# Performance work log

Hardware: AMD Instinct MI355X
Metric: run time of the kernel (lower is better)

## Reference

```python
import jax, jax.numpy as jnp
import numpy as np
import math

H = 16
DQ = 64
NEG = -1000000000.0


def setup_inputs() -> dict:
    key = jax.random.key(0)
    ks = jax.random.split(key, 8)
    B, S, D = 2, 2048, 1024
    scale = 1.0 / math.sqrt(D)
    return {
        "embedding": jax.random.normal(ks[0], (B, S, D), dtype=jnp.float32),
        "mask": jax.random.randint(ks[1], (B, 1, S), 0, 2, dtype=jnp.int32),
        "Wq": jax.random.normal(ks[2], (D, D), dtype=jnp.float32) * scale,
        "bq": jnp.zeros((D,), dtype=jnp.float32),
        "Wk": jax.random.normal(ks[3], (D, D), dtype=jnp.float32) * scale,
        "bk": jnp.zeros((D,), dtype=jnp.float32),
        "Wv": jax.random.normal(ks[4], (D, D), dtype=jnp.float32) * scale,
        "bv": jnp.zeros((D,), dtype=jnp.float32),
        "Wo": jax.random.normal(ks[5], (D, D), dtype=jnp.float32) * scale,
        "bo": jnp.zeros((D,), dtype=jnp.float32),
    }


def reference(embedding, mask, Wq, bq, Wk, bk, Wv, bv, Wo, bo):
    B, S, D = embedding.shape
    # projections -> [B, H, S, DQ]
    def proj(W, b):
        return (embedding @ W + b).reshape(B, S, H, DQ).transpose(0, 2, 1, 3)
    q, k, v = proj(Wq, bq), proj(Wk, bk), proj(Wv, bv)
    scores = jnp.einsum("bhqd,bhkd->bhqk", q, k) / math.sqrt(DQ)
    m = mask[:, None]  # [B,1,1,S] broadcasts over heads and query positions
    scores = jnp.where(m == 0, NEG, scores)
    attn = jax.nn.softmax(scores, axis=-1)
    x = jnp.einsum("bhqk,bhkd->bhqd", attn, v)
    x = x.transpose(0, 2, 1, 3).reshape(B, S, H * DQ)
    return x @ Wo + bo
```

## Files before the change

### kernel.cpp

```cpp
#include <hip/hip_runtime.h>
#include <stdint.h>

#define B_ 2
#define S_ 2048
#define D_ 1024
#define H_ 16
#define DQ_ 64
#define M_ 4096
#define CLOG2 16.0f

typedef unsigned short ushort_t;
typedef __attribute__((ext_vector_type(8))) short short8;
typedef __attribute__((ext_vector_type(4))) float floatx4;
typedef __attribute__((ext_vector_type(16))) float floatx16;

#if __has_builtin(__builtin_amdgcn_exp2f)
#define EXP2(x) __builtin_amdgcn_exp2f(x)
#else
#define EXP2(x) exp2f(x)
#endif

__device__ __forceinline__ ushort_t f2bf(float f) {
  union { float f; uint32_t u; } v; v.f = f;
  uint32_t r = v.u + 0x7FFFu + ((v.u >> 16) & 1u);
  return (ushort_t)(r >> 16);
}

__device__ __forceinline__ uint32_t pk2_trunc(float a, float b) {
  union { float f; uint32_t u; } va, vb; va.f = a; vb.f = b;
  return (va.u >> 16) | (vb.u & 0xFFFF0000u);
}
__device__ __forceinline__ uint32_t pk2_rne(float a, float b) {
  return (uint32_t)f2bf(a) | ((uint32_t)f2bf(b) << 16);
}

__device__ __forceinline__ void async16(const ushort_t* g, ushort_t* l) {
  __builtin_amdgcn_global_load_lds(
      (const __attribute__((address_space(1))) uint32_t*)g,
      (__attribute__((address_space(3))) uint32_t*)l, 16, 0, 0);
}


__global__ void k_cvt_emb(const float* __restrict__ in, ushort_t* __restrict__ out) {
  int i = (blockIdx.x * 256 + threadIdx.x) * 4;
  float4 v = *(const float4*)(in + i);
  uint64_t pk = (uint64_t)f2bf(v.x) | ((uint64_t)f2bf(v.y) << 16) |
                ((uint64_t)f2bf(v.z) << 32) | ((uint64_t)f2bf(v.w) << 48);
  *(uint64_t*)(out + i) = pk;
}

__global__ void k_cvt_w(const float* __restrict__ Wq, const float* __restrict__ Wk,
                        const float* __restrict__ Wv, const float* __restrict__ Wo,
                        ushort_t* __restrict__ Wt) {
  const float* W = (blockIdx.z == 0) ? Wq : (blockIdx.z == 1) ? Wk
                 : (blockIdx.z == 2) ? Wv : Wo;
  ushort_t* out = Wt + (size_t)blockIdx.z * D_ * D_;
  __shared__ float t[32][33];
  int k0 = blockIdx.x * 32, n0 = blockIdx.y * 32;
  int tx = threadIdx.x, ty = threadIdx.y;
  for (int r = 0; r < 32; r += 8)
    t[ty + r][tx] = W[(size_t)(k0 + ty + r) * D_ + n0 + tx];
  __syncthreads();
  for (int r = 0; r < 32; r += 8)
    out[(size_t)(n0 + ty + r) * D_ + k0 + tx] = f2bf(t[tx][ty + r]);
}

__global__ void k_cvt_mask(const int* __restrict__ mask, uint64_t* __restrict__ mbits) {
  int b = blockIdx.y, tile = blockIdx.x, lane = threadIdx.x;
  unsigned long long w = __ballot(mask[b * S_ + tile * 64 + lane] != 0);
  if (lane == 0) mbits[b * 32 + tile] = w;
}

template <int IM>
__device__ __forceinline__ void gemm_core2(const ushort_t* __restrict__ A,
                                           const ushort_t* __restrict__ Bt,
                                           ushort_t* As, ushort_t* Bs,
                                           int m0, int n0, floatx4 (&acc)[IM][4]) {
  int t = threadIdx.x, lane = t & 63, w = t >> 6;
  int wm = (w >> 1) * (IM * 16), wn = (w & 1) * 64;
  int l15 = lane & 15, quad = lane >> 4;
  int srow8 = (lane >> 3) & 7;
  int sch = ((lane & 7) ^ srow8) * 8;
  const ushort_t* Ag = A + (size_t)(m0 + w * 8 + srow8) * D_ + sch;
  const ushort_t* Bg = Bt + (size_t)(n0 + w * 8 + srow8) * D_ + sch;
  for (int kt = 0; kt < D_; kt += 64) {
    __syncthreads();
#pragma unroll
    for (int c = 0; c < IM; c++)
      async16(Ag + kt + (size_t)c * 32 * D_, As + (c * 32 + w * 8) * 64);
#pragma unroll
    for (int c = 0; c < 4; c++)
      async16(Bg + kt + (size_t)c * 32 * D_, Bs + (c * 32 + w * 8) * 64);
    __syncthreads();
#pragma unroll
    for (int ks = 0; ks < 2; ks++) {
      int ch = ((ks * 4 + quad) ^ (l15 & 7)) * 8;
      short8 a[IM], b[4];
#pragma unroll
      for (int i = 0; i < IM; i++)
        a[i] = *(const short8*)(As + (wm + i * 16 + l15) * 64 + ch);
#pragma unroll
      for (int j = 0; j < 4; j++)
        b[j] = *(const short8*)(Bs + (wn + j * 16 + l15) * 64 + ch);
#pragma unroll
      for (int i = 0; i < IM; i++)
#pragma unroll
        for (int j = 0; j < 4; j++)
          acc[i][j] = __builtin_amdgcn_mfma_f32_16x16x32_bf16(a[i], b[j], acc[i][j], 0, 0, 0);
    }
  }
}

__global__ __launch_bounds__(256, 3) void k_proj(
    const ushort_t* __restrict__ A, const ushort_t* __restrict__ Wt,
    const float* __restrict__ bq, const float* __restrict__ bk,
    const float* __restrict__ bv,
    ushort_t* __restrict__ Q, ushort_t* __restrict__ K, ushort_t* __restrict__ V) {
  __shared__ __align__(16) ushort_t As[128 * 64];
  __shared__ __align__(16) ushort_t Bs[128 * 64];
  int z = blockIdx.z;
  const ushort_t* Bt = Wt + (size_t)z * D_ * D_;
  const float* bias = (z == 0) ? bq : (z == 1) ? bk : bv;
  int m0 = blockIdx.x * 128, n0 = blockIdx.y * 128;
  floatx4 acc[4][4] = {};
  gemm_core2<4>(A, Bt, As, Bs, m0, n0, acc);
  int lane = threadIdx.x & 63, w = threadIdx.x >> 6;
  int wm = (w >> 1) * 64, wn = (w & 1) * 64;
  int quad = lane >> 4, l15 = lane & 15;
  float scale = (z == 0) ? 0.125f * 1.44269504f : 1.0f;
#pragma unroll
  for (int i = 0; i < 4; i++)
#pragma unroll
    for (int j = 0; j < 4; j++) {
      int ncol = n0 + wn + j * 16 + l15;
      float bb = bias[ncol];
      int h = ncol >> 6, dq = ncol & 63;
      int m = m0 + wm + i * 16 + quad * 4;
      int b = m >> 11, s = m & (S_ - 1);
      if (z == 2) {
        uint64_t pk = (uint64_t)f2bf(acc[i][j][0] + bb) |
                      ((uint64_t)f2bf(acc[i][j][1] + bb) << 16) |
                      ((uint64_t)f2bf(acc[i][j][2] + bb) << 32) |
                      ((uint64_t)f2bf(acc[i][j][3] + bb) << 48);
        *(uint64_t*)(V + ((size_t)(b * H_ + h) * DQ_ + dq) * S_ + s) = pk;
      } else {
        ushort_t* dst = (z == 0) ? Q : K;
#pragma unroll
        for (int r = 0; r < 4; r++)
          dst[((size_t)(b * H_ + h) * S_ + (s + r)) * DQ_ + dq] =
              f2bf((acc[i][j][r] + bb) * scale);
      }
    }
}

__global__ __launch_bounds__(256, 2) void k_attn(
    const ushort_t* __restrict__ Q, const ushort_t* __restrict__ Kg,
    const ushort_t* __restrict__ Vt, const uint64_t* __restrict__ mbits,
    ushort_t* __restrict__ X) {
  int bh = blockIdx.y, b = bh >> 4, h = bh & 15;
  int t = threadIdx.x, lane = t & 63, w = t >> 6;
  int l31 = lane & 31, hi = lane >> 5;
  int q0 = blockIdx.x * 128 + w * 32;
  const ushort_t* Qh = Q + (size_t)bh * S_ * DQ_;
  const ushort_t* Kh = Kg + (size_t)bh * S_ * DQ_;
  const ushort_t* Vh = Vt + (size_t)bh * DQ_ * S_;
  const uint64_t* mbp = mbits + b * 32;

  __shared__ __align__(16) ushort_t Ks[64 * 64];
  __shared__ __align__(16) ushort_t Vs[64 * 64];

  short8 qf[4];
#pragma unroll
  for (int ks = 0; ks < 4; ks++)
    qf[ks] = *(const short8*)(Qh + (size_t)(q0 + l31) * DQ_ + ks * 16 + hi * 8);

  int srow8 = (lane >> 3) & 7;
  int sch = ((lane & 7) ^ srow8) * 8;
  const ushort_t* Kg1 = Kh + (size_t)(w * 8 + srow8) * DQ_ + sch;
  const ushort_t* Vg1 = Vh + (size_t)(w * 8 + srow8) * S_ + sch;

  floatx16 o[2] = {};
  float lsum = 0.0f;

  for (int k0 = 0; k0 < S_; k0 += 64) {
    __syncthreads();
    async16(Kg1 + (size_t)k0 * DQ_, Ks + w * 512);
    async16(Kg1 + (size_t)(k0 + 32) * DQ_, Ks + w * 512 + 2048);
    async16(Vg1 + k0, Vs + w * 512);
    async16(Vg1 + (size_t)32 * S_ + k0, Vs + w * 512 + 2048);
    __syncthreads();

    floatx16 s0 = {}, s1 = {};
#pragma unroll
    for (int ks = 0; ks < 4; ks++) {
      int ch = ((ks * 2 + hi) ^ (l31 & 7)) * 8;
      short8 kf0 = *(const short8*)(Ks + l31 * 64 + ch);
      short8 kf1 = *(const short8*)(Ks + (32 + l31) * 64 + ch);
      s0 = __builtin_amdgcn_mfma_f32_32x32x16_bf16(kf0, qf[ks], s0, 0, 0, 0);
      s1 = __builtin_amdgcn_mfma_f32_32x32x16_bf16(kf1, qf[ks], s1, 0, 0, 0);
    }

    uint64_t mb64 = mbp[k0 >> 6];
    uint32_t pk[2][4][2];
#pragma unroll
    for (int g = 0; g < 4; g++) {
      float p0[4], p1[4];
#pragma unroll
      for (int j = 0; j < 4; j++) {
        int r = g * 4 + j;
        uint64_t sh = mb64 >> (8 * g + j + 4 * hi);
        p0[j] = (sh & 1) ? EXP2(s0[r] - CLOG2) : 0.0f;
        p1[j] = ((sh >> 32) & 1) ? EXP2(s1[r] - CLOG2) : 0.0f;
        lsum += p0[j] + p1[j];
      }
      pk[0][g][0] = pk2_trunc(p0[0], p0[1]); pk[0][g][1] = pk2_trunc(p0[2], p0[3]);
      pk[1][g][0] = pk2_trunc(p1[0], p1[1]); pk[1][g][1] = pk2_trunc(p1[2], p1[3]);
    }

#pragma unroll
    for (int ks = 0; ks < 4; ks++) {
      int a = ks >> 1, gb = (ks & 1) * 2;
      uint32_t pass0 = hi ? pk[a][gb][0]     : pk[a][gb + 1][0];
      uint32_t pass1 = hi ? pk[a][gb][1]     : pk[a][gb + 1][1];
      uint32_t own0  = hi ? pk[a][gb + 1][0] : pk[a][gb][0];
      uint32_t own1  = hi ? pk[a][gb + 1][1] : pk[a][gb][1];
      uint32_t recv0 = __shfl_xor(pass0, 32, 64);
      uint32_t recv1 = __shfl_xor(pass1, 32, 64);
      union { uint32_t u[4]; short8 v; } pf;
      pf.u[0] = hi ? recv0 : own0;
      pf.u[1] = hi ? recv1 : own1;
      pf.u[2] = hi ? own0 : recv0;
      pf.u[3] = hi ? own1 : recv1;
      int ch = ((ks * 2 + hi) ^ (l31 & 7)) * 8;
      short8 vf0 = *(const short8*)(Vs + l31 * 64 + ch);
      short8 vf1 = *(const short8*)(Vs + (32 + l31) * 64 + ch);
      o[0] = __builtin_amdgcn_mfma_f32_32x32x16_bf16(vf0, pf.v, o[0], 0, 0, 0);
      o[1] = __builtin_amdgcn_mfma_f32_32x32x16_bf16(vf1, pf.v, o[1], 0, 0, 0);
    }
  }

  float l = lsum + __shfl_xor(lsum, 32, 64);
  float inv = 1.0f / l;
  int q = q0 + l31;
  size_t base = (size_t)(b * S_ + q) * D_ + h * DQ_;
#pragma unroll
  for (int a = 0; a < 2; a++)
#pragma unroll
    for (int g = 0; g < 4; g++) {
      uint2 st;
      st.x = pk2_rne(o[a][4 * g] * inv, o[a][4 * g + 1] * inv);
      st.y = pk2_rne(o[a][4 * g + 2] * inv, o[a][4 * g + 3] * inv);
      *(uint2*)(X + base + a * 32 + g * 8 + 4 * hi) = st;
    }
}

__global__ __launch_bounds__(256, 2) void k_oproj(
    const ushort_t* __restrict__ A, const ushort_t* __restrict__ Wt,
    const float* __restrict__ bias, float* __restrict__ C) {
  __shared__ __align__(16) ushort_t As[64 * 64];
  __shared__ __align__(16) ushort_t Bs[128 * 64];
  int m0 = blockIdx.x * 64, n0 = blockIdx.y * 128;
  floatx4 acc[2][4] = {};
  gemm_core2<2>(A, Wt, As, Bs, m0, n0, acc);
  int lane = threadIdx.x & 63, w = threadIdx.x >> 6;
  int wm = (w >> 1) * 32, wn = (w & 1) * 64;
  int quad = lane >> 4, l15 = lane & 15;
#pragma unroll
  for (int i = 0; i < 2; i++)
#pragma unroll
    for (int j = 0; j < 4; j++) {
      int ncol = n0 + wn + j * 16 + l15;
      float bb = bias[ncol];
      int mr = m0 + wm + i * 16 + quad * 4;
#pragma unroll
      for (int r = 0; r < 4; r++)
        C[(size_t)(mr + r) * D_ + ncol] = acc[i][j][r] + bb;
    }
}

extern "C" void kernel_launch(void* const* d_in, const int* in_sizes, int n_in,
                              void* d_out, int out_size, void* d_ws, size_t ws_size,
                              hipStream_t stream) {
  const float* emb  = (const float*)d_in[0];
  const int*   mask = (const int*)d_in[1];
  const float* Wq = (const float*)d_in[2];
  const float* bq = (const float*)d_in[3];
  const float* Wk = (const float*)d_in[4];
  const float* bk = (const float*)d_in[5];
  const float* Wv = (const float*)d_in[6];
  const float* bv = (const float*)d_in[7];
  const float* Wo = (const float*)d_in[8];
  const float* bo = (const float*)d_in[9];
  float* out = (float*)d_out;

  ushort_t* embb = (ushort_t*)d_ws;
  ushort_t* Wt   = embb + (size_t)M_ * D_;
  ushort_t* Qb   = Wt + (size_t)4 * D_ * D_;
  ushort_t* Kb   = Qb + (size_t)M_ * D_;
  ushort_t* Vb   = Kb + (size_t)M_ * D_;
  ushort_t* Xb   = Vb + (size_t)M_ * D_;
  uint64_t* Mb   = (uint64_t*)(Xb + (size_t)M_ * D_);

  k_cvt_emb<<<dim3(M_ * D_ / 1024), 256, 0, stream>>>(emb, embb);
  k_cvt_w<<<dim3(32, 32, 4), dim3(32, 8), 0, stream>>>(Wq, Wk, Wv, Wo, Wt);
  k_cvt_mask<<<dim3(32, 2), 64, 0, stream>>>(mask, Mb);
  k_proj<<<dim3(32, 8, 3), 256, 0, stream>>>(embb, Wt, bq, bk, bv, Qb, Kb, Vb);
  k_attn<<<dim3(16, 32), 256, 0, stream>>>(Qb, Kb, Vb, Mb, Xb);
  k_oproj<<<dim3(64, 8), 256, 0, stream>>>(Xb, Wt + (size_t)3 * D_ * D_, bo, out);
}
```

Before: 205.6 us.

## Fold mask into extra MFMA bias and load K/V fragments directly from global

Replaces the per-element mask bit test and constant subtraction in the attention softmax with a bf16 additive bias per key (-16 for valid keys, a large negative value for masked ones). The bias is injected into the score accumulator by an extra MFMA that multiplies a one-hot query vector against it. K and V fragments are now read from global memory straight into registers, dropping the LDS staging and both __syncthreads per tile. This removes barrier and select overhead, at the cost of two extra MFMAs per tile, redundant uncoalesced global/L2 reads across the four waves, and reliance on exp2 underflowing to zero for masked keys.

```diff
diff --git a/kernel.cpp b/kernel.cpp
--- a/kernel.cpp
+++ b/kernel.cpp
@@ -7,7 +7,6 @@
 #define H_ 16
 #define DQ_ 64
 #define M_ 4096
-#define CLOG2 16.0f
 
 typedef unsigned short ushort_t;
 typedef __attribute__((ext_vector_type(8))) short short8;
@@ -65,10 +64,9 @@
     out[(size_t)(n0 + ty + r) * D_ + k0 + tx] = f2bf(t[tx][ty + r]);
 }
 
-__global__ void k_cvt_mask(const int* __restrict__ mask, uint64_t* __restrict__ mbits) {
-  int b = blockIdx.y, tile = blockIdx.x, lane = threadIdx.x;
-  unsigned long long w = __ballot(mask[b * S_ + tile * 64 + lane] != 0);
-  if (lane == 0) mbits[b * 32 + tile] = w;
+__global__ void k_cvt_bias(const int* __restrict__ mask, ushort_t* __restrict__ biasK) {
+  int i = blockIdx.x * 256 + threadIdx.x;
+  biasK[i] = mask[i] ? 0xC180 : 0xCE6E;
 }
 
 template <int IM>
@@ -155,7 +153,7 @@
 
 __global__ __launch_bounds__(256, 2) void k_attn(
     const ushort_t* __restrict__ Q, const ushort_t* __restrict__ Kg,
-    const ushort_t* __restrict__ Vt, const uint64_t* __restrict__ mbits,
+    const ushort_t* __restrict__ Vt, const ushort_t* __restrict__ biasK,
     ushort_t* __restrict__ X) {
   int bh = blockIdx.y, b = bh >> 4, h = bh & 15;
   int t = threadIdx.x, lane = t & 63, w = t >> 6;
@@ -164,53 +162,55 @@
   const ushort_t* Qh = Q + (size_t)bh * S_ * DQ_;
   const ushort_t* Kh = Kg + (size_t)bh * S_ * DQ_;
   const ushort_t* Vh = Vt + (size_t)bh * DQ_ * S_;
-  const uint64_t* mbp = mbits + b * 32;
-
-  __shared__ __align__(16) ushort_t Ks[64 * 64];
-  __shared__ __align__(16) ushort_t Vs[64 * 64];
+  const ushort_t* bbp = biasK + b * S_;
 
   short8 qf[4];
 #pragma unroll
   for (int ks = 0; ks < 4; ks++)
     qf[ks] = *(const short8*)(Qh + (size_t)(q0 + l31) * DQ_ + ks * 16 + hi * 8);
 
-  int srow8 = (lane >> 3) & 7;
-  int sch = ((lane & 7) ^ srow8) * 8;
-  const ushort_t* Kg1 = Kh + (size_t)(w * 8 + srow8) * DQ_ + sch;
-  const ushort_t* Vg1 = Vh + (size_t)(w * 8 + srow8) * S_ + sch;
+  short8 qb = {};
+  qb[0] = hi ? (short)0 : (short)0x3F80;
+
+  const ushort_t* Kp0 = Kh + (size_t)l31 * DQ_ + hi * 8;
+  const ushort_t* Kp1 = Kh + (size_t)(32 + l31) * DQ_ + hi * 8;
+  const ushort_t* Vp0 = Vh + (size_t)l31 * S_ + hi * 8;
+  const ushort_t* Vp1 = Vh + (size_t)(32 + l31) * S_ + hi * 8;
 
   floatx16 o[2] = {};
   float lsum = 0.0f;
 
   for (int k0 = 0; k0 < S_; k0 += 64) {
-    __syncthreads();
-    async16(Kg1 + (size_t)k0 * DQ_, Ks + w * 512);
-    async16(Kg1 + (size_t)(k0 + 32) * DQ_, Ks + w * 512 + 2048);
-    async16(Vg1 + k0, Vs + w * 512);
-    async16(Vg1 + (size_t)32 * S_ + k0, Vs + w * 512 + 2048);
-    __syncthreads();
+    short8 kf0[4], kf1[4], vf0[4], vf1[4];
+#pragma unroll
+    for (int ks = 0; ks < 4; ks++) {
+      kf0[ks] = *(const short8*)(Kp0 + (size_t)k0 * DQ_ + ks * 16);
+      kf1[ks] = *(const short8*)(Kp1 + (size_t)k0 * DQ_ + ks * 16);
+      vf0[ks] = *(const short8*)(Vp0 + k0 + ks * 16);
+      vf1[ks] = *(const short8*)(Vp1 + k0 + ks * 16);
+    }
+    ushort_t bv0 = bbp[k0 + l31], bv1 = bbp[k0 + 32 + l31];
+    short8 kb0 = {}, kb1 = {};
+    kb0[0] = hi ? (short)0 : (short)bv0;
+    kb1[0] = hi ? (short)0 : (short)bv1;
 
     floatx16 s0 = {}, s1 = {};
 #pragma unroll
     for (int ks = 0; ks < 4; ks++) {
-      int ch = ((ks * 2 + hi) ^ (l31 & 7)) * 8;
-      short8 kf0 = *(const short8*)(Ks + l31 * 64 + ch);
-      short8 kf1 = *(const short8*)(Ks + (32 + l31) * 64 + ch);
-      s0 = __builtin_amdgcn_mfma_f32_32x32x16_bf16(kf0, qf[ks], s0, 0, 0, 0);
-      s1 = __builtin_amdgcn_mfma_f32_32x32x16_bf16(kf1, qf[ks], s1, 0, 0, 0);
-    }
-
-    uint64_t mb64 = mbp[k0 >> 6];
+      s0 = __builtin_amdgcn_mfma_f32_32x32x16_bf16(kf0[ks], qf[ks], s0, 0, 0, 0);
+      s1 = __builtin_amdgcn_mfma_f32_32x32x16_bf16(kf1[ks], qf[ks], s1, 0, 0, 0);
+    }
+    s0 = __builtin_amdgcn_mfma_f32_32x32x16_bf16(kb0, qb, s0, 0, 0, 0);
+    s1 = __builtin_amdgcn_mfma_f32_32x32x16_bf16(kb1, qb, s1, 0, 0, 0);
+
     uint32_t pk[2][4][2];
 #pragma unroll
     for (int g = 0; g < 4; g++) {
       float p0[4], p1[4];
 #pragma unroll
       for (int j = 0; j < 4; j++) {
-        int r = g * 4 + j;
-        uint64_t sh = mb64 >> (8 * g + j + 4 * hi);
-        p0[j] = (sh & 1) ? EXP2(s0[r] - CLOG2) : 0.0f;
-        p1[j] = ((sh >> 32) & 1) ? EXP2(s1[r] - CLOG2) : 0.0f;
+        p0[j] = EXP2(s0[g * 4 + j]);
+        p1[j] = EXP2(s1[g * 4 + j]);
         lsum += p0[j] + p1[j];
       }
       pk[0][g][0] = pk2_trunc(p0[0], p0[1]); pk[0][g][1] = pk2_trunc(p0[2], p0[3]);
@@ -231,11 +231,8 @@
       pf.u[1] = hi ? recv1 : own1;
       pf.u[2] = hi ? own0 : recv0;
       pf.u[3] = hi ? own1 : recv1;
-      int ch = ((ks * 2 + hi) ^ (l31 & 7)) * 8;
-      short8 vf0 = *(const short8*)(Vs + l31 * 64 + ch);
-      short8 vf1 = *(const short8*)(Vs + (32 + l31) * 64 + ch);
-      o[0] = __builtin_amdgcn_mfma_f32_32x32x16_bf16(vf0, pf.v, o[0], 0, 0, 0);
-      o[1] = __builtin_amdgcn_mfma_f32_32x32x16_bf16(vf1, pf.v, o[1], 0, 0, 0);
+      o[0] = __builtin_amdgcn_mfma_f32_32x32x16_bf16(vf0[ks], pf.v, o[0], 0, 0, 0);
+      o[1] = __builtin_amdgcn_mfma_f32_32x32x16_bf16(vf1[ks], pf.v, o[1], 0, 0, 0);
     }
   }
 
@@ -299,12 +296,12 @@
   ushort_t* Kb   = Qb + (size_t)M_ * D_;
   ushort_t* Vb   = Kb + (size_t)M_ * D_;
   ushort_t* Xb   = Vb + (size_t)M_ * D_;
-  uint64_t* Mb   = (uint64_t*)(Xb + (size_t)M_ * D_);
+  ushort_t* Bi   = Xb + (size_t)M_ * D_;
 
   k_cvt_emb<<<dim3(M_ * D_ / 1024), 256, 0, stream>>>(emb, embb);
   k_cvt_w<<<dim3(32, 32, 4), dim3(32, 8), 0, stream>>>(Wq, Wk, Wv, Wo, Wt);
-  k_cvt_mask<<<dim3(32, 2), 64, 0, stream>>>(mask, Mb);
+  k_cvt_bias<<<dim3(B_ * S_ / 256), 256, 0, stream>>>(mask, Bi);
   k_proj<<<dim3(32, 8, 3), 256, 0, stream>>>(embb, Wt, bq, bk, bv, Qb, Kb, Vb);
-  k_attn<<<dim3(16, 32), 256, 0, stream>>>(Qb, Kb, Vb, Mb, Xb);
+  k_attn<<<dim3(16, 32), 256, 0, stream>>>(Qb, Kb, Vb, Bi, Xb);
   k_oproj<<<dim3(64, 8), 256, 0, stream>>>(Xb, Wt + (size_t)3 * D_ * D_, bo, out);
 }
```

Result: slower. 262.0 us (+27.4%).

## Compact unmasked keys/values and loop attention only over valid key count

Applied to the files above, without the earlier changes.

Adds a per-batch prefix scan over the mask that gives each unmasked position a compacted index and a padded key count. The K/V projection epilogue scatters rows to those compacted positions, and attention loops only up to the valid count, skipping fully masked key tiles. Per-key masking and the constant shift are folded into an extra bias MFMA using a padding bias vector, so the per-element select logic goes away. The cost is a serial single-wave scan kernel, scattered stores in the projection, and one extra MFMA per tile. Padding slots rely on a large negative bias to give near-zero weights.

```diff
diff --git a/kernel.cpp b/kernel.cpp
--- a/kernel.cpp
+++ b/kernel.cpp
@@ -7,7 +7,6 @@
 #define H_ 16
 #define DQ_ 64
 #define M_ 4096
-#define CLOG2 16.0f
 
 typedef unsigned short ushort_t;
 typedef __attribute__((ext_vector_type(8))) short short8;
@@ -65,10 +64,24 @@
     out[(size_t)(n0 + ty + r) * D_ + k0 + tx] = f2bf(t[tx][ty + r]);
 }
 
-__global__ void k_cvt_mask(const int* __restrict__ mask, uint64_t* __restrict__ mbits) {
-  int b = blockIdx.y, tile = blockIdx.x, lane = threadIdx.x;
-  unsigned long long w = __ballot(mask[b * S_ + tile * 64 + lane] != 0);
-  if (lane == 0) mbits[b * 32 + tile] = w;
+__global__ void k_mask_scan(const int* __restrict__ mask, int* __restrict__ pos,
+                            ushort_t* __restrict__ biasC, int* __restrict__ cntp) {
+  int b = blockIdx.x, lane = threadIdx.x;
+  int base = 0;
+  for (int c = 0; c < 32; c++) {
+    int s = c * 64 + lane;
+    bool m = mask[b * S_ + s] != 0;
+    unsigned long long bits = __ballot(m);
+    int pre = base + __popcll(bits & ((1ull << lane) - 1ull));
+    pos[b * S_ + s] = m ? pre : -1;
+    base += __popcll(bits);
+  }
+  int cnt = base;
+  for (int c = 0; c < 32; c++) {
+    int i = c * 64 + lane;
+    biasC[b * S_ + i] = (i < cnt) ? (ushort_t)0xC180 : (ushort_t)0xCE6E;
+  }
+  if (lane == 0) cntp[b] = (cnt + 63) & ~63;
 }
 
 template <int IM>
@@ -114,7 +127,7 @@
 __global__ __launch_bounds__(256, 3) void k_proj(
     const ushort_t* __restrict__ A, const ushort_t* __restrict__ Wt,
     const float* __restrict__ bq, const float* __restrict__ bk,
-    const float* __restrict__ bv,
+    const float* __restrict__ bv, const int* __restrict__ pos,
     ushort_t* __restrict__ Q, ushort_t* __restrict__ K, ushort_t* __restrict__ V) {
   __shared__ __align__(16) ushort_t As[128 * 64];
   __shared__ __align__(16) ushort_t Bs[128 * 64];
@@ -127,7 +140,7 @@
   int lane = threadIdx.x & 63, w = threadIdx.x >> 6;
   int wm = (w >> 1) * 64, wn = (w & 1) * 64;
   int quad = lane >> 4, l15 = lane & 15;
-  float scale = (z == 0) ? 0.125f * 1.44269504f : 1.0f;
+  float scale = 0.125f * 1.44269504f;
 #pragma unroll
   for (int i = 0; i < 4; i++)
 #pragma unroll
@@ -137,34 +150,39 @@
       int h = ncol >> 6, dq = ncol & 63;
       int m = m0 + wm + i * 16 + quad * 4;
       int b = m >> 11, s = m & (S_ - 1);
-      if (z == 2) {
-        uint64_t pk = (uint64_t)f2bf(acc[i][j][0] + bb) |
-                      ((uint64_t)f2bf(acc[i][j][1] + bb) << 16) |
-                      ((uint64_t)f2bf(acc[i][j][2] + bb) << 32) |
-                      ((uint64_t)f2bf(acc[i][j][3] + bb) << 48);
-        *(uint64_t*)(V + ((size_t)(b * H_ + h) * DQ_ + dq) * S_ + s) = pk;
+      if (z == 0) {
+#pragma unroll
+        for (int r = 0; r < 4; r++)
+          Q[((size_t)(b * H_ + h) * S_ + (s + r)) * DQ_ + dq] =
+              f2bf((acc[i][j][r] + bb) * scale);
       } else {
-        ushort_t* dst = (z == 0) ? Q : K;
-#pragma unroll
-        for (int r = 0; r < 4; r++)
-          dst[((size_t)(b * H_ + h) * S_ + (s + r)) * DQ_ + dq] =
-              f2bf((acc[i][j][r] + bb) * scale);
+        int4 p4 = *(const int4*)(pos + b * S_ + s);
+#pragma unroll
+        for (int r = 0; r < 4; r++) {
+          int ps = (&p4.x)[r];
+          if (ps >= 0) {
+            float v = acc[i][j][r] + bb;
+            if (z == 1) K[((size_t)(b * H_ + h) * S_ + ps) * DQ_ + dq] = f2bf(v);
+            else        V[((size_t)(b * H_ + h) * DQ_ + dq) * S_ + ps] = f2bf(v);
+          }
+        }
       }
     }
 }
 
 __global__ __launch_bounds__(256, 2) void k_attn(
-    const ushort_t* __restrict__ Q, const ushort_t* __restrict__ Kg,
-    const ushort_t* __restrict__ Vt, const uint64_t* __restrict__ mbits,
-    ushort_t* __restrict__ X) {
+    const ushort_t* __restrict__ Q, const ushort_t* __restrict__ Kc,
+    const ushort_t* __restrict__ Vc, const ushort_t* __restrict__ biasC,
+    const int* __restrict__ cntp, ushort_t* __restrict__ X) {
   int bh = blockIdx.y, b = bh >> 4, h = bh & 15;
   int t = threadIdx.x, lane = t & 63, w = t >> 6;
   int l31 = lane & 31, hi = lane >> 5;
   int q0 = blockIdx.x * 128 + w * 32;
   const ushort_t* Qh = Q + (size_t)bh * S_ * DQ_;
-  const ushort_t* Kh = Kg + (size_t)bh * S_ * DQ_;
-  const ushort_t* Vh = Vt + (size_t)bh * DQ_ * S_;
-  const uint64_t* mbp = mbits + b * 32;
+  const ushort_t* Kh = Kc + (size_t)bh * S_ * DQ_;
+  const ushort_t* Vh = Vc + (size_t)bh * DQ_ * S_;
+  const ushort_t* bbp = biasC + b * S_;
+  int nk = cntp[b];
 
   __shared__ __align__(16) ushort_t Ks[64 * 64];
   __shared__ __align__(16) ushort_t Vs[64 * 64];
@@ -173,6 +191,9 @@
 #pragma unroll
   for (int ks = 0; ks < 4; ks++)
     qf[ks] = *(const short8*)(Qh + (size_t)(q0 + l31) * DQ_ + ks * 16 + hi * 8);
+
+  short8 qb = {};
+  qb[0] = hi ? (short)0 : (short)0x3F80;
 
   int srow8 = (lane >> 3) & 7;
   int sch = ((lane & 7) ^ srow8) * 8;
@@ -182,12 +203,13 @@
   floatx16 o[2] = {};
   float lsum = 0.0f;
 
-  for (int k0 = 0; k0 < S_; k0 += 64) {
+  for (int k0 = 0; k0 < nk; k0 += 64) {
     __syncthreads();
     async16(Kg1 + (size_t)k0 * DQ_, Ks + w * 512);
     async16(Kg1 + (size_t)(k0 + 32) * DQ_, Ks + w * 512 + 2048);
     async16(Vg1 + k0, Vs + w * 512);
     async16(Vg1 + (size_t)32 * S_ + k0, Vs + w * 512 + 2048);
+    ushort_t bv0 = bbp[k0 + l31], bv1 = bbp[k0 + 32 + l31];
     __syncthreads();
 
     floatx16 s0 = {}, s1 = {};
@@ -199,18 +221,20 @@
       s0 = __builtin_amdgcn_mfma_f32_32x32x16_bf16(kf0, qf[ks], s0, 0, 0, 0);
       s1 = __builtin_amdgcn_mfma_f32_32x32x16_bf16(kf1, qf[ks], s1, 0, 0, 0);
     }
-
-    uint64_t mb64 = mbp[k0 >> 6];
+    short8 kb0 = {}, kb1 = {};
+    kb0[0] = hi ? (short)0 : (short)bv0;
+    kb1[0] = hi ? (short)0 : (short)bv1;
+    s0 = __builtin_amdgcn_mfma_f32_32x32x16_bf16(kb0, qb, s0, 0, 0, 0);
+    s1 = __builtin_amdgcn_mfma_f32_32x32x16_bf16(kb1, qb, s1, 0, 0, 0);
+
     uint32_t pk[2][4][2];
 #pragma unroll
     for (int g = 0; g < 4; g++) {
       float p0[4], p1[4];
 #pragma unroll
       for (int j = 0; j < 4; j++) {
-        int r = g * 4 + j;
-        uint64_t sh = mb64 >> (8 * g + j + 4 * hi);
-        p0[j] = (sh & 1) ? EXP2(s0[r] - CLOG2) : 0.0f;
-        p1[j] = ((sh >> 32) & 1) ? EXP2(s1[r] - CLOG2) : 0.0f;
+        p0[j] = EXP2(s0[g * 4 + j]);
+        p1[j] = EXP2(s1[g * 4 + j]);
         lsum += p0[j] + p1[j];
       }
       pk[0][g][0] = pk2_trunc(p0[0], p0[1]); pk[0][g][1] = pk2_trunc(p0[2], p0[3]);
@@ -293,18 +317,20 @@
   const float* bo = (const float*)d_in[9];
   float* out = (float*)d_out;
 
-  ushort_t* embb = (ushort_t*)d_ws;
-  ushort_t* Wt   = embb + (size_t)M_ * D_;
-  ushort_t* Qb   = Wt + (size_t)4 * D_ * D_;
-  ushort_t* Kb   = Qb + (size_t)M_ * D_;
-  ushort_t* Vb   = Kb + (size_t)M_ * D_;
-  ushort_t* Xb   = Vb + (size_t)M_ * D_;
-  uint64_t* Mb   = (uint64_t*)(Xb + (size_t)M_ * D_);
+  ushort_t* embb  = (ushort_t*)d_ws;
+  ushort_t* Wt    = embb + (size_t)M_ * D_;
+  ushort_t* Qb    = Wt + (size_t)4 * D_ * D_;
+  ushort_t* Kb    = Qb + (size_t)M_ * D_;
+  ushort_t* Vb    = Kb + (size_t)M_ * D_;
+  ushort_t* Xb    = Vb + (size_t)M_ * D_;
+  ushort_t* biasC = Xb + (size_t)M_ * D_;
+  int* pos        = (int*)(biasC + (size_t)B_ * S_);
+  int* cntp       = pos + B_ * S_;
 
   k_cvt_emb<<<dim3(M_ * D_ / 1024), 256, 0, stream>>>(emb, embb);
   k_cvt_w<<<dim3(32, 32, 4), dim3(32, 8), 0, stream>>>(Wq, Wk, Wv, Wo, Wt);
-  k_cvt_mask<<<dim3(32, 2), 64, 0, stream>>>(mask, Mb);
-  k_proj<<<dim3(32, 8, 3), 256, 0, stream>>>(embb, Wt, bq, bk, bv, Qb, Kb, Vb);
-  k_attn<<<dim3(16, 32), 256, 0, stream>>>(Qb, Kb, Vb, Mb, Xb);
+  k_mask_scan<<<dim3(B_), 64, 0, stream>>>(mask, pos, biasC, cntp);
+  k_proj<<<dim3(32, 8, 3), 256, 0, stream>>>(embb, Wt, bq, bk, bv, pos, Qb, Kb, Vb);
+  k_attn<<<dim3(16, 32), 256, 0, stream>>>(Qb, Kb, Vb, biasC, cntp, Xb);
   k_oproj<<<dim3(64, 8), 256, 0, stream>>>(Xb, Wt + (size_t)3 * D_ * D_, bo, out);
 }
```

New measurement: 186.3 us. 1.1x faster.
